# Performance work log

Hardware: AMD Instinct MI355X
Metric: run time of the kernel (lower is better)

Reference implementation:

```python
import jax, jax.numpy as jnp
import numpy as np

N = 8192        # nodes (A.shape[0])
D_IN = 128      # input_dim
D_OUT = 128     # output_dim
D_THETA = 256   # hardcoded in GCN_liner_theta_1
DROP_KEEP = 0.8 # DropEdge percent


def setup_inputs() -> dict:
    key = jax.random.key(0)
    ks = jax.random.split(key, 6)
    H = jax.random.normal(ks[0], (N, D_IN), dtype=jnp.float32)
    U = jax.random.uniform(ks[1], (N, N), dtype=jnp.float32)
    upper = jnp.triu((U < 0.01).astype(jnp.float32), 1)
    A_adj = upper + upper.T + jnp.eye(N, dtype=jnp.float32)
    bn_gamma = jnp.ones((D_IN,), jnp.float32)
    bn_beta = jnp.zeros((D_IN,), jnp.float32)
    W_theta = jax.random.normal(ks[2], (D_THETA, D_IN), jnp.float32) * 0.05
    b_theta = jnp.zeros((D_THETA,), jnp.float32)
    W_out = jax.random.normal(ks[3], (D_OUT, D_IN), jnp.float32) * 0.05
    b_out = jnp.zeros((D_OUT,), jnp.float32)
    return {"H": H, "A_adj": A_adj, "bn_gamma": bn_gamma, "bn_beta": bn_beta,
            "W_theta": W_theta, "b_theta": b_theta, "W_out": W_out, "b_out": b_out}


def reference(H, A_adj, bn_gamma, bn_beta, W_theta, b_theta, W_out, b_out):
    n = H.shape[0]
    # BatchNorm1d in training mode: batch stats over the node dimension
    mean = H.mean(axis=0)
    var = H.var(axis=0)  # biased, matches torch training normalization
    Hn = (H - mean) * jax.lax.rsqrt(var + 1e-5) * bn_gamma + bn_beta

    # theta projection -> pairwise euclidean distances
    Hx = Hn @ W_theta.T + b_theta                     # [N, 256]
    sq = jnp.sum(Hx * Hx, axis=1)                     # [N]
    dist = sq[:, None] + sq[None, :] - 2.0 * (Hx @ Hx.T)
    dist = jnp.sqrt(jnp.clip(dist, 1e-12, None))      # [N, N]

    A = jnp.exp(-0.2 * dist)
    A = jnp.clip(jax.nn.sigmoid(A), 0.1, None)
    # DropEdge detaches A in the original (A never carries grad)
    A = jax.lax.stop_gradient(A)

    dkey = jax.random.key(42)
    keep = jax.random.uniform(dkey, (n, n)) < DROP_KEEP
    triu = jnp.triu(jnp.ones((n, n), dtype=bool), 0)
    Bt = jnp.where(triu & keep, A, 0.0)
    B = Bt + Bt.T - jnp.diag(jnp.diag(Bt))

    mask = jnp.ceil(A_adj * 1e-5)
    A2 = B * mask + jnp.eye(n, dtype=B.dtype)
    A3 = jnp.where(A2 > 0.6, A2, 0.0)                 # threshold (host loop in torch)

    # symmetric normalization D^-1/2 A D^-1/2 without dense diag matmuls
    d_inv_sqrt = jax.lax.rsqrt(A3.sum(axis=1))        # diag always >= 1
    A_hat = A3 * d_inv_sqrt[:, None] * d_inv_sqrt[None, :]

    out = A_hat @ (Hn @ W_out.T + b_out)              # [N, D_OUT]
    out = jnp.where(out >= 0, out, 0.01 * out)        # LeakyReLU(0.01)
    return out, A3
```

## Files before the change

### kernel.cpp

```cpp
#include <hip/hip_runtime.h>
#include <cstdint>
#include <cstddef>

#define N 8192
#define DIN 128
#define DTH 256
#define DOUT 128
#define ROWCAP 256
#define LISTCAP 512

__device__ __forceinline__ void threefry_0_42(uint32_t x0, uint32_t x1,
                                              uint32_t& o0, uint32_t& o1) {
  const uint32_t ks0 = 0u;
  const uint32_t ks1 = 42u;
  const uint32_t ks2 = 0x1BD11BDAu ^ 0u ^ 42u;
  x0 += ks0; x1 += ks1;
#define TF_R(r) { x0 += x1; x1 = (x1 << (r)) | (x1 >> (32 - (r))); x1 ^= x0; }
  TF_R(13) TF_R(15) TF_R(26) TF_R(6)
  x0 += ks1; x1 += ks2 + 1u;
  TF_R(17) TF_R(29) TF_R(16) TF_R(24)
  x0 += ks2; x1 += ks0 + 2u;
  TF_R(13) TF_R(15) TF_R(26) TF_R(6)
  x0 += ks0; x1 += ks1 + 3u;
  TF_R(17) TF_R(29) TF_R(16) TF_R(24)
  x0 += ks1; x1 += ks2 + 4u;
  TF_R(13) TF_R(15) TF_R(26) TF_R(6)
  x0 += ks2; x1 += ks0 + 5u;
#undef TF_R
  o0 = x0; o1 = x1;
}

__device__ __forceinline__ bool dropedge_keep(uint32_t t) {
  uint32_t y0, y1;
  threefry_0_42(0u, t, y0, y1);
  uint32_t bits = y0 ^ y1;
  float u = __uint_as_float((bits >> 9) | 0x3f800000u) - 1.0f;
  return u < 0.8f;
}

__global__ __launch_bounds__(256) void k_zero(float4* __restrict__ A3) {
  size_t idx = (size_t)blockIdx.x * 256 + threadIdx.x;
  const float4 z = make_float4(0.f, 0.f, 0.f, 0.f);
#pragma unroll
  for (int it = 0; it < 8; ++it)
    A3[idx + (size_t)it * 8192 * 256] = z;
}

__global__ __launch_bounds__(256) void k_bn_part(const float* __restrict__ H,
                                                 float* __restrict__ part_s,
                                                 float* __restrict__ part_s2) {
  __shared__ float ls[8][DIN];
  __shared__ float ls2[8][DIN];
  int tid = threadIdx.x;
  int rg = tid >> 5;
  int c4 = tid & 31;
  int rbase = blockIdx.x * 128;
  float s[4] = {0,0,0,0}, s2[4] = {0,0,0,0};
  for (int k = 0; k < 16; ++k) {
    int r = rbase + rg + k * 8;
    float4 h = ((const float4*)(H + (size_t)r * DIN))[c4];
    s[0] += h.x; s2[0] += h.x * h.x;
    s[1] += h.y; s2[1] += h.y * h.y;
    s[2] += h.z; s2[2] += h.z * h.z;
    s[3] += h.w; s2[3] += h.w * h.w;
  }
#pragma unroll
  for (int q = 0; q < 4; ++q) { ls[rg][c4*4+q] = s[q]; ls2[rg][c4*4+q] = s2[q]; }
  __syncthreads();
  if (tid < DIN) {
    float a = 0.f, b = 0.f;
#pragma unroll
    for (int g = 0; g < 8; ++g) { a += ls[g][tid]; b += ls2[g][tid]; }
    part_s[blockIdx.x * DIN + tid] = a;
    part_s2[blockIdx.x * DIN + tid] = b;
  }
}

__global__ void k_bn_final(const float* __restrict__ part_s,
                           const float* __restrict__ part_s2,
                           const float* __restrict__ gamma,
                           const float* __restrict__ beta,
                           float* __restrict__ scale,
                           float* __restrict__ shift) {
  int c = threadIdx.x;
  float s = 0.f, s2 = 0.f;
  for (int b = 0; b < 64; ++b) { s += part_s[b*DIN+c]; s2 += part_s2[b*DIN+c]; }
  float mean = s * (1.0f / N);
  float var  = s2 * (1.0f / N) - mean * mean;
  float sc = rsqrtf(var + 1e-5f) * gamma[c];
  scale[c] = sc;
  shift[c] = beta[c] - mean * sc;
}

__global__ void k_prep(const float* __restrict__ Wt, const float* __restrict__ bt,
                       const float* __restrict__ Wo, const float* __restrict__ bo,
                       float* __restrict__ Wc, float* __restrict__ bc) {
  int idx = blockIdx.x * 256 + threadIdx.x;
  if (blockIdx.x < 192) {
    int k = idx / 384, c = idx % 384;
    Wc[idx] = (c < 256) ? Wt[(size_t)c * DIN + k] : Wo[(size_t)(c - 256) * DIN + k];
  } else {
    int c = idx - 192 * 256;
    if (c < 384) bc[c] = (c < 256) ? bt[c] : bo[c - 256];
  }
}

__global__ __launch_bounds__(256) void k_rows(
    const float* __restrict__ H, const float* __restrict__ scale,
    const float* __restrict__ shift, const float* __restrict__ Wc,
    const float* __restrict__ bc, float* __restrict__ Hx,
    float* __restrict__ HW, float* __restrict__ sq) {
  __shared__ float hn[16][DIN];
  int tid = threadIdx.x;
  int base = blockIdx.x * 16;
#pragma unroll
  for (int k = 0; k < 2; ++k) {
    int f = tid + k * 256;
    int r = f >> 5, c4 = f & 31;
    float4 h  = ((const float4*)(H + (size_t)(base + r) * DIN))[c4];
    float4 sc = ((const float4*)scale)[c4];
    float4 sh = ((const float4*)shift)[c4];
    h.x = h.x * sc.x + sh.x; h.y = h.y * sc.y + sh.y;
    h.z = h.z * sc.z + sh.z; h.w = h.w * sc.w + sh.w;
    ((float4*)hn[r])[c4] = h;
  }
  __syncthreads();
  int w = tid >> 6, lane = tid & 63;
  int r0 = w * 4;
  float acc[4][6];
#pragma unroll
  for (int r = 0; r < 4; ++r)
#pragma unroll
    for (int q = 0; q < 6; ++q) acc[r][q] = 0.f;

  for (int k4 = 0; k4 < 32; ++k4) {
    float4 h[4];
#pragma unroll
    for (int r = 0; r < 4; ++r) h[r] = ((const float4*)hn[r0 + r])[k4];
#pragma unroll
    for (int kk = 0; kk < 4; ++kk) {
      const float* wrow = Wc + (size_t)(k4 * 4 + kk) * 384 + lane;
      float wv[6];
#pragma unroll
      for (int q = 0; q < 6; ++q) wv[q] = wrow[64 * q];
#pragma unroll
      for (int r = 0; r < 4; ++r) {
        float hs = (kk == 0) ? h[r].x : (kk == 1) ? h[r].y
                 : (kk == 2) ? h[r].z : h[r].w;
#pragma unroll
        for (int q = 0; q < 6; ++q) acc[r][q] += hs * wv[q];
      }
    }
  }
#pragma unroll
  for (int r = 0; r < 4; ++r) {
    int row = base + r0 + r;
    float s = 0.f;
#pragma unroll
    for (int q = 0; q < 4; ++q) {
      float v = acc[r][q] + bc[lane + 64 * q];
      Hx[(size_t)row * DTH + lane + 64 * q] = v;
      s += v * v;
    }
#pragma unroll
    for (int off = 32; off > 0; off >>= 1) s += __shfl_xor(s, off, 64);
    if (lane == 0) sq[row] = s;
#pragma unroll
    for (int q = 4; q < 6; ++q) {
      float v = acc[r][q] + bc[lane + 64 * q];
      HW[(size_t)row * DOUT + lane + 64 * (q - 4)] = v;
    }
  }
}

__global__ __launch_bounds__(256) void k_edges(
    const float* __restrict__ A_adj, const float* __restrict__ Hx,
    const float* __restrict__ sq,
    float* __restrict__ deg, int* __restrict__ nnz_cnt,
    int* __restrict__ nnz_idx, float* __restrict__ nnz_val) {
  __shared__ float hx_i[DTH];
  __shared__ int   s_list[LISTCAP];
  __shared__ int   s_cnt;
  __shared__ float s_deg;
  __shared__ int   s_nnz;
  int i = blockIdx.x;
  int tid = threadIdx.x;
  if (tid == 0) { s_cnt = 0; s_deg = 0.f; s_nnz = 0; }
  hx_i[tid] = Hx[(size_t)i * DTH + tid];
  __syncthreads();

  const float4* arow = (const float4*)(A_adj + (size_t)i * N);
  float4 a[8];
#pragma unroll
  for (int it = 0; it < 8; ++it) a[it] = arow[tid + it * 256];
#pragma unroll
  for (int it = 0; it < 8; ++it) {
    float av[4] = {a[it].x, a[it].y, a[it].z, a[it].w};
    int j = (tid + it * 256) * 4;
#pragma unroll
    for (int q = 0; q < 4; ++q) {
      if (av[q] != 0.f) {
        int p = atomicAdd(&s_cnt, 1);
        if (p < LISTCAP) s_list[p] = j + q;
      }
    }
  }
  __syncthreads();

  int M = min(s_cnt, LISTCAP);
  float sqi = sq[i];
  for (int t = tid; t < M; t += 256) {
    int j = s_list[t];
    uint32_t r = (uint32_t)min(i, j), c = (uint32_t)max(i, j);
    bool keep = dropedge_keep(r * (uint32_t)N + c);
    const float4* hj = (const float4*)(Hx + (size_t)j * DTH);
    float dot = 0.f;
#pragma unroll 8
    for (int c4 = 0; c4 < DTH / 4; ++c4) {
      float4 h = hj[c4];
      dot += h.x * hx_i[c4*4+0] + h.y * hx_i[c4*4+1]
           + h.z * hx_i[c4*4+2] + h.w * hx_i[c4*4+3];
    }
    float dist = sqi + sq[j] - 2.0f * dot;
    dist = sqrtf(fmaxf(dist, 1e-12f));
    float aval = expf(-0.2f * dist);
    float sg = 1.0f / (1.0f + expf(-aval));
    sg = fmaxf(sg, 0.1f);
    float b = keep ? sg : 0.0f;
    float a2 = b + ((i == j) ? 1.0f : 0.0f);
    float a3v = (a2 > 0.6f) ? a2 : 0.0f;
    if (a3v != 0.f) {
      atomicAdd(&s_deg, a3v);
      int p = atomicAdd(&s_nnz, 1);
      if (p < ROWCAP) {
        nnz_idx[(size_t)i * ROWCAP + p] = j;
        nnz_val[(size_t)i * ROWCAP + p] = a3v;
      }
    }
  }
  __syncthreads();
  if (tid == 0) { deg[i] = s_deg; nnz_cnt[i] = min(s_nnz, ROWCAP); }
}

__global__ __launch_bounds__(256) void k_scatter(
    const int* __restrict__ nnz_cnt, const int* __restrict__ nnz_idx,
    const float* __restrict__ nnz_val, float* __restrict__ A3) {
  int i = blockIdx.x * 256 + threadIdx.x;
  if (i >= N) return;
  int cnt = nnz_cnt[i];
  for (int e = 0; e < cnt; ++e)
    A3[(size_t)i * N + nnz_idx[(size_t)i * ROWCAP + e]] =
        nnz_val[(size_t)i * ROWCAP + e];
}

__global__ __launch_bounds__(128) void k_out(
    const float* __restrict__ HW, const float* __restrict__ deg,
    const int* __restrict__ nnz_cnt, const int* __restrict__ nnz_idx,
    const float* __restrict__ nnz_val, float* __restrict__ out) {
  int i = blockIdx.x;
  int c = threadIdx.x;
  int cnt = nnz_cnt[i];
  float acc = 0.f;
  for (int e = 0; e < cnt; ++e) {
    int j = nnz_idx[(size_t)i * ROWCAP + e];
    float v = nnz_val[(size_t)i * ROWCAP + e];
    acc += v * rsqrtf(deg[j]) * HW[(size_t)j * DOUT + c];
  }
  float o = rsqrtf(deg[i]) * acc;
  out[(size_t)i * DOUT + c] = (o >= 0.f) ? o : 0.01f * o;
}

extern "C" void kernel_launch(void* const* d_in, const int* in_sizes, int n_in,
                              void* d_out, int out_size, void* d_ws, size_t ws_size,
                              hipStream_t stream) {
  const float* H     = (const float*)d_in[0];
  const float* A_adj = (const float*)d_in[1];
  const float* gamma = (const float*)d_in[2];
  const float* beta  = (const float*)d_in[3];
  const float* Wt    = (const float*)d_in[4];
  const float* bt    = (const float*)d_in[5];
  const float* Wo    = (const float*)d_in[6];
  const float* bo    = (const float*)d_in[7];

  float* out = (float*)d_out;
  float* A3  = out + (size_t)N * DOUT;

  float* ws    = (float*)d_ws;
  float* scale = ws;
  float* shift = ws + 128;
  float* Hx    = ws + 256;
  float* sq    = Hx + (size_t)N * DTH;
  float* HW    = sq + N;
  float* deg   = HW + (size_t)N * DOUT;
  int*   nnz_cnt = (int*)(deg + N);
  int*   nnz_idx = nnz_cnt + N;
  float* nnz_val = (float*)(nnz_idx + (size_t)N * ROWCAP);
  float* part_s  = nnz_val + (size_t)N * ROWCAP;
  float* part_s2 = part_s + 64 * DIN;
  float* Wc      = part_s2 + 64 * DIN;
  float* bc      = Wc + 128 * 384;

  k_zero<<<8192, 256, 0, stream>>>((float4*)A3);
  k_bn_part<<<64, 256, 0, stream>>>(H, part_s, part_s2);
  k_bn_final<<<1, DIN, 0, stream>>>(part_s, part_s2, gamma, beta, scale, shift);
  k_prep<<<194, 256, 0, stream>>>(Wt, bt, Wo, bo, Wc, bc);
  k_rows<<<N / 16, 256, 0, stream>>>(H, scale, shift, Wc, bc, Hx, HW, sq);
  k_edges<<<N, 256, 0, stream>>>(A_adj, Hx, sq, deg, nnz_cnt, nnz_idx, nnz_val);
  k_scatter<<<32, 256, 0, stream>>>(nnz_cnt, nnz_idx, nnz_val, A3);
  k_out<<<N, DOUT, 0, stream>>>(HW, deg, nnz_cnt, nnz_idx, nnz_val, out);
}
```

Before: 546.7 us.

## Exploit adjacency symmetry, store Hx as bf16, and fuse zeroing and scatter kernels

```diff
diff --git a/kernel.cpp b/kernel.cpp
--- a/kernel.cpp
+++ b/kernel.cpp
@@ -38,41 +38,50 @@
   return u < 0.8f;
 }
 
-__global__ __launch_bounds__(256) void k_zero(float4* __restrict__ A3) {
-  size_t idx = (size_t)blockIdx.x * 256 + threadIdx.x;
-  const float4 z = make_float4(0.f, 0.f, 0.f, 0.f);
-#pragma unroll
-  for (int it = 0; it < 8; ++it)
-    A3[idx + (size_t)it * 8192 * 256] = z;
-}
-
-__global__ __launch_bounds__(256) void k_bn_part(const float* __restrict__ H,
-                                                 float* __restrict__ part_s,
-                                                 float* __restrict__ part_s2) {
-  __shared__ float ls[8][DIN];
-  __shared__ float ls2[8][DIN];
+__global__ __launch_bounds__(256) void k_pre(
+    const float* __restrict__ H,
+    const float* __restrict__ Wt, const float* __restrict__ bt,
+    const float* __restrict__ Wo, const float* __restrict__ bo,
+    float* __restrict__ part_s, float* __restrict__ part_s2,
+    float* __restrict__ Wc, float* __restrict__ bc,
+    float* __restrict__ deg ) {
+  int b = blockIdx.x;
   int tid = threadIdx.x;
-  int rg = tid >> 5;
-  int c4 = tid & 31;
-  int rbase = blockIdx.x * 128;
-  float s[4] = {0,0,0,0}, s2[4] = {0,0,0,0};
-  for (int k = 0; k < 16; ++k) {
-    int r = rbase + rg + k * 8;
-    float4 h = ((const float4*)(H + (size_t)r * DIN))[c4];
-    s[0] += h.x; s2[0] += h.x * h.x;
-    s[1] += h.y; s2[1] += h.y * h.y;
-    s[2] += h.z; s2[2] += h.z * h.z;
-    s[3] += h.w; s2[3] += h.w * h.w;
-  }
-#pragma unroll
-  for (int q = 0; q < 4; ++q) { ls[rg][c4*4+q] = s[q]; ls2[rg][c4*4+q] = s2[q]; }
-  __syncthreads();
-  if (tid < DIN) {
-    float a = 0.f, b = 0.f;
-#pragma unroll
-    for (int g = 0; g < 8; ++g) { a += ls[g][tid]; b += ls2[g][tid]; }
-    part_s[blockIdx.x * DIN + tid] = a;
-    part_s2[blockIdx.x * DIN + tid] = b;
+  if (b < 64) {
+    __shared__ float ls[8][DIN];
+    __shared__ float ls2[8][DIN];
+    int rg = tid >> 5;
+    int c4 = tid & 31;
+    int rbase = b * 128;
+    float s[4] = {0,0,0,0}, s2[4] = {0,0,0,0};
+    for (int k = 0; k < 16; ++k) {
+      int r = rbase + rg + k * 8;
+      float4 h = ((const float4*)(H + (size_t)r * DIN))[c4];
+      s[0] += h.x; s2[0] += h.x * h.x;
+      s[1] += h.y; s2[1] += h.y * h.y;
+      s[2] += h.z; s2[2] += h.z * h.z;
+      s[3] += h.w; s2[3] += h.w * h.w;
+    }
+#pragma unroll
+    for (int q = 0; q < 4; ++q) { ls[rg][c4*4+q] = s[q]; ls2[rg][c4*4+q] = s2[q]; }
+    __syncthreads();
+    if (tid < DIN) {
+      float a = 0.f, bb = 0.f;
+#pragma unroll
+      for (int g = 0; g < 8; ++g) { a += ls[g][tid]; bb += ls2[g][tid]; }
+      part_s[b * DIN + tid] = a;
+      part_s2[b * DIN + tid] = bb;
+    }
+  } else if (b < 256) {
+    int idx = (b - 64) * 256 + tid;
+    int k = idx / 384, c = idx % 384;
+    Wc[idx] = (c < 256) ? Wt[(size_t)c * DIN + k] : Wo[(size_t)(c - 256) * DIN + k];
+  } else if (b < 258) {
+    int c = (b - 256) * 256 + tid;
+    if (c < 384) bc[c] = (c < 256) ? bt[c] : bo[c - 256];
+  } else {
+    int g = (b - 258) * 256 + tid;
+    ((int4*)deg)[g] = make_int4(0, 0, 0, 0);
   }
 }
 
@@ -92,23 +101,16 @@
   shift[c] = beta[c] - mean * sc;
 }
 
-__global__ void k_prep(const float* __restrict__ Wt, const float* __restrict__ bt,
-                       const float* __restrict__ Wo, const float* __restrict__ bo,
-                       float* __restrict__ Wc, float* __restrict__ bc) {
-  int idx = blockIdx.x * 256 + threadIdx.x;
-  if (blockIdx.x < 192) {
-    int k = idx / 384, c = idx % 384;
-    Wc[idx] = (c < 256) ? Wt[(size_t)c * DIN + k] : Wo[(size_t)(c - 256) * DIN + k];
-  } else {
-    int c = idx - 192 * 256;
-    if (c < 384) bc[c] = (c < 256) ? bt[c] : bo[c - 256];
-  }
+__device__ __forceinline__ unsigned short f2bf(float v) {
+  uint32_t u = __float_as_uint(v);
+  u += 0x7fffu + ((u >> 16) & 1u);
+  return (unsigned short)(u >> 16);
 }
 
 __global__ __launch_bounds__(256) void k_rows(
     const float* __restrict__ H, const float* __restrict__ scale,
     const float* __restrict__ shift, const float* __restrict__ Wc,
-    const float* __restrict__ bc, float* __restrict__ Hx,
+    const float* __restrict__ bc, unsigned short* __restrict__ Hxh,
     float* __restrict__ HW, float* __restrict__ sq) {
   __shared__ float hn[16][DIN];
   int tid = threadIdx.x;
@@ -159,7 +161,7 @@
 #pragma unroll
     for (int q = 0; q < 4; ++q) {
       float v = acc[r][q] + bc[lane + 64 * q];
-      Hx[(size_t)row * DTH + lane + 64 * q] = v;
+      Hxh[(size_t)row * DTH + lane + 64 * q] = f2bf(v);
       s += v * v;
     }
 #pragma unroll
@@ -173,35 +175,40 @@
   }
 }
 
-__global__ __launch_bounds__(256) void k_edges(
-    const float* __restrict__ A_adj, const float* __restrict__ Hx,
-    const float* __restrict__ sq,
+__global__ __launch_bounds__(256) void k_main(
+    const float* __restrict__ A_adj, const unsigned short* __restrict__ Hxh,
+    const float* __restrict__ sq, float* __restrict__ A3,
     float* __restrict__ deg, int* __restrict__ nnz_cnt,
     int* __restrict__ nnz_idx, float* __restrict__ nnz_val) {
-  __shared__ float hx_i[DTH];
+  int b = blockIdx.x;
+  int tid = threadIdx.x;
+  if (b < 8192) {
+    float4* row = (float4*)(A3 + (size_t)b * N);
+    const float4 z = make_float4(0.f, 0.f, 0.f, 0.f);
+#pragma unroll
+    for (int it = 0; it < 8; ++it) row[tid + it * 256] = z;
+    return;
+  }
+  int i = b - 8192;
+  __shared__ float4 hx4[64];
   __shared__ int   s_list[LISTCAP];
   __shared__ int   s_cnt;
-  __shared__ float s_deg;
-  __shared__ int   s_nnz;
-  int i = blockIdx.x;
-  int tid = threadIdx.x;
-  if (tid == 0) { s_cnt = 0; s_deg = 0.f; s_nnz = 0; }
-  hx_i[tid] = Hx[(size_t)i * DTH + tid];
+  if (tid == 0) s_cnt = 0;
+  ((float*)hx4)[tid] = __uint_as_float(((uint32_t)Hxh[(size_t)i * DTH + tid]) << 16);
   __syncthreads();
 
   const float4* arow = (const float4*)(A_adj + (size_t)i * N);
-  float4 a[8];
-#pragma unroll
-  for (int it = 0; it < 8; ++it) a[it] = arow[tid + it * 256];
-#pragma unroll
-  for (int it = 0; it < 8; ++it) {
-    float av[4] = {a[it].x, a[it].y, a[it].z, a[it].w};
-    int j = (tid + it * 256) * 4;
+  int q0 = i >> 2;
+  for (int q4 = q0 + tid; q4 < N / 4; q4 += 256) {
+    float4 a = arow[q4];
+    int jb = q4 * 4;
+    float av[4] = {a.x, a.y, a.z, a.w};
 #pragma unroll
     for (int q = 0; q < 4; ++q) {
-      if (av[q] != 0.f) {
+      int j = jb + q;
+      if (av[q] != 0.f && j >= i) {
         int p = atomicAdd(&s_cnt, 1);
-        if (p < LISTCAP) s_list[p] = j + q;
+        if (p < LISTCAP) s_list[p] = j;
       }
     }
   }
@@ -211,55 +218,63 @@
   float sqi = sq[i];
   for (int t = tid; t < M; t += 256) {
     int j = s_list[t];
-    uint32_t r = (uint32_t)min(i, j), c = (uint32_t)max(i, j);
-    bool keep = dropedge_keep(r * (uint32_t)N + c);
-    const float4* hj = (const float4*)(Hx + (size_t)j * DTH);
-    float dot = 0.f;
+    bool keep = dropedge_keep((uint32_t)i * (uint32_t)N + (uint32_t)j);
+    float dist;
+    if (j == i) {
+      dist = 1e-6f;
+    } else {
+      const uint4* hj = (const uint4*)(Hxh + (size_t)j * DTH);
+      float dot = 0.f;
 #pragma unroll 8
-    for (int c4 = 0; c4 < DTH / 4; ++c4) {
-      float4 h = hj[c4];
-      dot += h.x * hx_i[c4*4+0] + h.y * hx_i[c4*4+1]
-           + h.z * hx_i[c4*4+2] + h.w * hx_i[c4*4+3];
-    }
-    float dist = sqi + sq[j] - 2.0f * dot;
-    dist = sqrtf(fmaxf(dist, 1e-12f));
+      for (int c = 0; c < 32; ++c) {
+        uint4 u = hj[c];
+        float4 f0 = hx4[2 * c], f1 = hx4[2 * c + 1];
+        dot += __uint_as_float(u.x << 16) * f0.x
+             + __uint_as_float(u.x & 0xffff0000u) * f0.y
+             + __uint_as_float(u.y << 16) * f0.z
+             + __uint_as_float(u.y & 0xffff0000u) * f0.w
+             + __uint_as_float(u.z << 16) * f1.x
+             + __uint_as_float(u.z & 0xffff0000u) * f1.y
+             + __uint_as_float(u.w << 16) * f1.z
+             + __uint_as_float(u.w & 0xffff0000u) * f1.w;
+      }
+      dist = sqrtf(fmaxf(sqi + sq[j] - 2.0f * dot, 1e-12f));
+    }
     float aval = expf(-0.2f * dist);
-    float sg = 1.0f / (1.0f + expf(-aval));
-    sg = fmaxf(sg, 0.1f);
-    float b = keep ? sg : 0.0f;
-    float a2 = b + ((i == j) ? 1.0f : 0.0f);
+    float sg = fmaxf(1.0f / (1.0f + expf(-aval)), 0.1f);
+    float bb = keep ? sg : 0.0f;
+    float a2 = bb + ((i == j) ? 1.0f : 0.0f);
     float a3v = (a2 > 0.6f) ? a2 : 0.0f;
     if (a3v != 0.f) {
-      atomicAdd(&s_deg, a3v);
-      int p = atomicAdd(&s_nnz, 1);
+      atomicAdd(&deg[i], a3v);
+      int p = atomicAdd(&nnz_cnt[i], 1);
       if (p < ROWCAP) {
         nnz_idx[(size_t)i * ROWCAP + p] = j;
         nnz_val[(size_t)i * ROWCAP + p] = a3v;
       }
-    }
-  }
-  __syncthreads();
-  if (tid == 0) { deg[i] = s_deg; nnz_cnt[i] = min(s_nnz, ROWCAP); }
-}
-
-__global__ __launch_bounds__(256) void k_scatter(
+      if (j != i) {
+        atomicAdd(&deg[j], a3v);
+        int p2 = atomicAdd(&nnz_cnt[j], 1);
+        if (p2 < ROWCAP) {
+          nnz_idx[(size_t)j * ROWCAP + p2] = i;
+          nnz_val[(size_t)j * ROWCAP + p2] = a3v;
+        }
+      }
+    }
+  }
+}
+
+__global__ __launch_bounds__(128) void k_post(
+    const float* __restrict__ HW, const float* __restrict__ deg,
     const int* __restrict__ nnz_cnt, const int* __restrict__ nnz_idx,
-    const float* __restrict__ nnz_val, float* __restrict__ A3) {
-  int i = blockIdx.x * 256 + threadIdx.x;
-  if (i >= N) return;
-  int cnt = nnz_cnt[i];
-  for (int e = 0; e < cnt; ++e)
+    const float* __restrict__ nnz_val, float* __restrict__ A3,
+    float* __restrict__ out) {
+  int i = blockIdx.x;
+  int c = threadIdx.x;
+  int cnt = min(nnz_cnt[i], ROWCAP);
+  for (int e = c; e < cnt; e += 128)
     A3[(size_t)i * N + nnz_idx[(size_t)i * ROWCAP + e]] =
         nnz_val[(size_t)i * ROWCAP + e];
-}
-
-__global__ __launch_bounds__(128) void k_out(
-    const float* __restrict__ HW, const float* __restrict__ deg,
-    const int* __restrict__ nnz_cnt, const int* __restrict__ nnz_idx,
-    const float* __restrict__ nnz_val, float* __restrict__ out) {
-  int i = blockIdx.x;
-  int c = threadIdx.x;
-  int cnt = nnz_cnt[i];
   float acc = 0.f;
   for (int e = 0; e < cnt; ++e) {
     int j = nnz_idx[(size_t)i * ROWCAP + e];
@@ -288,8 +303,8 @@
   float* ws    = (float*)d_ws;
   float* scale = ws;
   float* shift = ws + 128;
-  float* Hx    = ws + 256;
-  float* sq    = Hx + (size_t)N * DTH;
+  unsigned short* Hxh = (unsigned short*)(ws + 256);
+  float* sq    = ws + 256 + (size_t)N * 128;
   float* HW    = sq + N;
   float* deg   = HW + (size_t)N * DOUT;
   int*   nnz_cnt = (int*)(deg + N);
@@ -300,12 +315,9 @@
   float* Wc      = part_s2 + 64 * DIN;
   float* bc      = Wc + 128 * 384;
 
-  k_zero<<<8192, 256, 0, stream>>>((float4*)A3);
-  k_bn_part<<<64, 256, 0, stream>>>(H, part_s, part_s2);
+  k_pre<<<274, 256, 0, stream>>>(H, Wt, bt, Wo, bo, part_s, part_s2, Wc, bc, deg);
   k_bn_final<<<1, DIN, 0, stream>>>(part_s, part_s2, gamma, beta, scale, shift);
-  k_prep<<<194, 256, 0, stream>>>(Wt, bt, Wo, bo, Wc, bc);
-  k_rows<<<N / 16, 256, 0, stream>>>(H, scale, shift, Wc, bc, Hx, HW, sq);
-  k_edges<<<N, 256, 0, stream>>>(A_adj, Hx, sq, deg, nnz_cnt, nnz_idx, nnz_val);
-  k_scatter<<<32, 256, 0, stream>>>(nnz_cnt, nnz_idx, nnz_val, A3);
-  k_out<<<N, DOUT, 0, stream>>>(HW, deg, nnz_cnt, nnz_idx, nnz_val, out);
-}
+  k_rows<<<N / 16, 256, 0, stream>>>(H, scale, shift, Wc, bc, Hxh, HW, sq);
+  k_main<<<2 * N, 256, 0, stream>>>(A_adj, Hxh, sq, A3, deg, nnz_cnt, nnz_idx, nnz_val);
+  k_post<<<N, DOUT, 0, stream>>>(HW, deg, nnz_cnt, nnz_idx, nnz_val, A3, out);
+}
```

Result: faster. 492.1 us (-10.0%).
